# Kernel optimization log

Measured on AMD Instinct MI355X. Metric: run time of the kernel, lower is better.

## Reference

```python
import jax, jax.numpy as jnp
import numpy as np

NUM_ITERATIONS = 3


def squash(t, axis=-1):
    # scale * t / ||t||, scale = ||t||^2 / (1 + ||t||^2)
    sq = jnp.sum(t * t, axis=axis, keepdims=True)
    return (sq / (1.0 + sq)) * t / jnp.sqrt(sq)


def setup_inputs() -> dict:
    key = jax.random.key(0)
    k1, k2 = jax.random.split(key)
    B, N_IN, IN_DIM = 32, 2048, 32
    N_OUT, OUT_DIM = 64, 32
    x = jax.random.normal(k1, (B, N_IN, IN_DIM), dtype=jnp.float32)
    weight = jax.random.normal(k2, (N_OUT, N_IN, OUT_DIM, IN_DIM), dtype=jnp.float32) * 0.05
    return {"x": x, "weight": weight}


def reference(x, weight):
    # u_hat[b,o,i,d] = sum_k W[o,i,d,k] * x[b,i,k]  -- prediction vectors
    u_hat = jnp.einsum('oidk,bik->boid', weight, x)  # [B, N_out, N_in, out_dim]
    b = jnp.zeros(u_hat.shape[:3] + (1,), dtype=u_hat.dtype)  # routing logits
    v = None
    for _ in range(NUM_ITERATIONS):
        c = jax.nn.softmax(b, axis=1)                      # over output capsules
        s = jnp.sum(c * u_hat, axis=2, keepdims=True)      # [B, N_out, 1, out_dim]
        v = squash(s, axis=-1)
        b = b + jnp.sum(u_hat * v, axis=-1, keepdims=True)  # agreement update
    return jnp.squeeze(v, axis=2)  # [B, N_out, out_dim]
```

## Files before the change

### kernel.cpp

```cpp
#include <hip/hip_runtime.h>

#define NI   2048
#define NO   64
#define DD   32
#define ODIM 2048

typedef short bf16x8 __attribute__((ext_vector_type(8)));
typedef float f32x4  __attribute__((ext_vector_type(4)));
typedef unsigned int u32x2 __attribute__((ext_vector_type(2)));
typedef unsigned int u32x4 __attribute__((ext_vector_type(4)));

__device__ __forceinline__ unsigned int cvt_pk_bf16(float lo, float hi) {
  unsigned int r;
  asm("v_cvt_pk_bf16_f32 %0, %1, %2" : "=v"(r) : "v"(lo), "v"(hi));
  return r;
}
__device__ __forceinline__ float bflo(unsigned int u) { return __uint_as_float(u << 16); }
__device__ __forceinline__ float bfhi(unsigned int u) { return __uint_as_float(u & 0xffff0000u); }

union BFPack { unsigned int u[4]; bf16x8 v; };

__global__ __launch_bounds__(256) void k1_uhat(
    const float* __restrict__ W, const float* __restrict__ X,
    unsigned short* __restrict__ U, float* __restrict__ part) {
  __shared__ __attribute__((aligned(16))) char olds[8 * 32 * 144];
  __shared__ __attribute__((aligned(16))) unsigned short xlds[8][32][32];
  const int tid   = threadIdx.x;
  const int lane  = tid & 63;
  const int w     = tid >> 6;
  const int ob    = blockIdx.x & 31;
  const int ib    = blockIdx.x >> 5;
  const int odq   = (ob << 2) + w;
  const int o     = odq >> 1;
  const int db    = (odq & 1) << 4;
  const int row16 = lane & 15;
  const int kg    = lane >> 4;
  const int k0    = kg << 3;
  const int crow  = kg << 2;
  const int ccol  = lane & 15;
  const int odl   = (w << 4) + crow;
  const int sb    = tid >> 3;
  const int sii   = tid & 7;
  const int xslot = (kg ^ (ccol & 3)) << 3;

  f32x4 sacc[2];
  sacc[0] = f32x4{0.f, 0.f, 0.f, 0.f};
  sacc[1] = f32x4{0.f, 0.f, 0.f, 0.f};

  const float* wbase = W + (((size_t)o * NI) << 10) + ((db + row16) << 5) + k0;

  auto STAGE = [&](int p) {
    const int i = (ib << 5) + (p << 3) + sii;
    const float4* xp = (const float4*)(X + (((size_t)(sb * NI + i)) << 5));
    float4 xv[8];
#pragma unroll
    for (int j = 0; j < 8; ++j) xv[j] = xp[j];
#pragma unroll
    for (int j = 0; j < 4; ++j) {
      u32x4 pk;
      pk.x = cvt_pk_bf16(xv[2*j].x,   xv[2*j].y);
      pk.y = cvt_pk_bf16(xv[2*j].z,   xv[2*j].w);
      pk.z = cvt_pk_bf16(xv[2*j+1].x, xv[2*j+1].y);
      pk.w = cvt_pk_bf16(xv[2*j+1].z, xv[2*j+1].w);
      *(u32x4*)&xlds[sii][sb][(j ^ (sb & 3)) << 3] = pk;
    }
  };

  auto ISSUE = [&](int p, int h, f32x4* wa, f32x4* wb) {
    const int ia = (ib << 5) + (p << 3) + (h << 2);
#pragma unroll
    for (int j = 0; j < 4; ++j) {
      const f32x4* wp = (const f32x4*)(wbase + ((size_t)(ia + j) << 10));
      wa[j] = __builtin_nontemporal_load(wp);
      wb[j] = __builtin_nontemporal_load(wp + 1);
    }
    __builtin_amdgcn_sched_barrier(0);
  };

  auto CONSUME = [&](int h, const f32x4* wa, const f32x4* wb) {
#pragma unroll
    for (int j = 0; j < 4; ++j) {
      const int ii = (h << 2) + j;
      bf16x8 bx0 = *(const bf16x8*)&xlds[ii][ccol][xslot];
      bf16x8 bx1 = *(const bf16x8*)&xlds[ii][ccol + 16][xslot];
      BFPack af;
      af.u[0] = cvt_pk_bf16(wa[j].x, wa[j].y);
      af.u[1] = cvt_pk_bf16(wa[j].z, wa[j].w);
      af.u[2] = cvt_pk_bf16(wb[j].x, wb[j].y);
      af.u[3] = cvt_pk_bf16(wb[j].z, wb[j].w);
      {
        f32x4 d = __builtin_amdgcn_mfma_f32_16x16x32_bf16(
            af.v, bx0, f32x4{0.f, 0.f, 0.f, 0.f}, 0, 0, 0);
        sacc[0] += d;
        u32x2 pk; pk.x = cvt_pk_bf16(d[0], d[1]); pk.y = cvt_pk_bf16(d[2], d[3]);
        *(u32x2*)(olds + ((ii << 5) + ccol) * 144 + (odl << 1)) = pk;
      }
      {
        f32x4 d = __builtin_amdgcn_mfma_f32_16x16x32_bf16(
            af.v, bx1, f32x4{0.f, 0.f, 0.f, 0.f}, 0, 0, 0);
        sacc[1] += d;
        u32x2 pk; pk.x = cvt_pk_bf16(d[0], d[1]); pk.y = cvt_pk_bf16(d[2], d[3]);
        *(u32x2*)(olds + ((ii << 5) + ccol + 16) * 144 + (odl << 1)) = pk;
      }
    }
  };

  f32x4 wa0[4], wb0[4], wa1[4], wb1[4];
  STAGE(0);
  ISSUE(0, 0, wa0, wb0);
  __syncthreads();

  for (int p = 0; p < 4; ++p) {
    const int i0 = (ib << 5) + (p << 3);
    ISSUE(p, 1, wa1, wb1);
    CONSUME(0, wa0, wb0);
    if (p < 3) ISSUE(p + 1, 0, wa0, wb0);
    CONSUME(1, wa1, wb1);
    __syncthreads();
    if (p < 3) STAGE(p + 1);
    {
      const int b    = tid >> 3;
      const int od16 = tid & 7;
#pragma unroll
      for (int r = 0; r < 8; ++r) {
        const u32x4 v = *(const u32x4*)(olds + ((r << 5) + b) * 144 + (od16 << 4));
        const size_t goff = (((size_t)(b * NI + i0 + r)) << 11) + (ob << 6) + (od16 << 3);
        *(u32x4*)(U + goff) = v;
      }
    }
    __syncthreads();
  }

#pragma unroll
  for (int bt = 0; bt < 2; ++bt) {
    const int b  = ccol + (bt << 4);
    const int od = (ob << 6) + odl;
    float* pp = part + (((size_t)((ib << 5) + b)) << 11) + od;
    float4 t; t.x = sacc[bt][0]; t.y = sacc[bt][1];
    t.z = sacc[bt][2]; t.w = sacc[bt][3];
    *(float4*)pp = t;
  }
}

__global__ __launch_bounds__(256) void k_reduce(
    const float* __restrict__ part, float* __restrict__ vout, float scale) {
  const int tid  = threadIdx.x;
  const int lane = tid & 63;
  const int wid  = (blockIdx.x << 2) + (tid >> 6);
  const int o = wid & 63, b = wid >> 6;
  const int d = lane & 31, h = lane >> 5;
  float s = 0.f;
  for (int c = h; c < 64; c += 2)
    s += part[(((size_t)((c << 5) + b)) << 11) + (o << 5) + d];
  s += __shfl_xor(s, 32);
  s *= scale;
  float p = s * s;
#pragma unroll
  for (int off = 1; off < 32; off <<= 1) p += __shfl_xor(p, off);
  const float v = (p > 0.f) ? s * sqrtf(p) / (1.f + p) : 0.f;
  if (h == 0) vout[(((b << 6) + o) << 5) + d] = v;
}

__global__ __launch_bounds__(256) void k_route(
    const unsigned short* __restrict__ U, const float* __restrict__ V1,
    const float* __restrict__ V2, float* __restrict__ part) {
  __shared__ float red[4][ODIM];
  const int tid   = threadIdx.x;
  const int lane  = tid & 63;
  const int w     = tid >> 6;
  const int b     = blockIdx.x >> 6;
  const int chunk = blockIdx.x & 63;
  const int o     = lane;

  float vs[32];
  {
    const float* vp = V1 + (((b << 6) + o) << 5);
#pragma unroll
    for (int j = 0; j < 8; ++j) {
      const float4 t = *(const float4*)(vp + (j << 2));
      vs[4*j+0] = t.x; vs[4*j+1] = t.y; vs[4*j+2] = t.z; vs[4*j+3] = t.w;
    }
    if (V2 != nullptr) {
      const float* vq = V2 + (((b << 6) + o) << 5);
#pragma unroll
      for (int j = 0; j < 8; ++j) {
        const float4 t = *(const float4*)(vq + (j << 2));
        vs[4*j+0] += t.x; vs[4*j+1] += t.y; vs[4*j+2] += t.z; vs[4*j+3] += t.w;
      }
    }
  }

  float pacc[32];
#pragma unroll
  for (int d = 0; d < 32; ++d) pacc[d] = 0.f;

  const int i0 = (chunk << 5) + (w << 3);
  const unsigned short* ub = U + (((size_t)b * NI) << 11);

  u32x4 q0, q1, q2, q3;
  {
    const u32x4* p = (const u32x4*)(ub + (((size_t)i0) << 11) + (o << 5));
    q0 = p[0]; q1 = p[1]; q2 = p[2]; q3 = p[3];
  }
  for (int ii = 0; ii < 8; ++ii) {
    const u32x4 c0 = q0, c1 = q1, c2 = q2, c3 = q3;
    if (ii < 7) {
      const u32x4* p = (const u32x4*)(ub + (((size_t)(i0 + ii + 1)) << 11) + (o << 5));
      q0 = p[0]; q1 = p[1]; q2 = p[2]; q3 = p[3];
    }
    float uf[32];
    uf[ 0]=bflo(c0.x); uf[ 1]=bfhi(c0.x); uf[ 2]=bflo(c0.y); uf[ 3]=bfhi(c0.y);
    uf[ 4]=bflo(c0.z); uf[ 5]=bfhi(c0.z); uf[ 6]=bflo(c0.w); uf[ 7]=bfhi(c0.w);
    uf[ 8]=bflo(c1.x); uf[ 9]=bfhi(c1.x); uf[10]=bflo(c1.y); uf[11]=bfhi(c1.y);
    uf[12]=bflo(c1.z); uf[13]=bfhi(c1.z); uf[14]=bflo(c1.w); uf[15]=bfhi(c1.w);
    uf[16]=bflo(c2.x); uf[17]=bfhi(c2.x); uf[18]=bflo(c2.y); uf[19]=bfhi(c2.y);
    uf[20]=bflo(c2.z); uf[21]=bfhi(c2.z); uf[22]=bflo(c2.w); uf[23]=bfhi(c2.w);
    uf[24]=bflo(c3.x); uf[25]=bfhi(c3.x); uf[26]=bflo(c3.y); uf[27]=bfhi(c3.y);
    uf[28]=bflo(c3.z); uf[29]=bfhi(c3.z); uf[30]=bflo(c3.w); uf[31]=bfhi(c3.w);

    float dotA = 0.f, dotB = 0.f;
#pragma unroll
    for (int d = 0; d < 16; ++d) {
      dotA = fmaf(uf[d], vs[d], dotA);
      dotB = fmaf(uf[d + 16], vs[d + 16], dotB);
    }
    const float dot = dotA + dotB;
    float m = dot;
#pragma unroll
    for (int off = 1; off < 64; off <<= 1) m = fmaxf(m, __shfl_xor(m, off));
    const float e = __expf(dot - m);
    float Z = e;
#pragma unroll
    for (int off = 1; off < 64; off <<= 1) Z += __shfl_xor(Z, off);
    const float c = e / Z;
#pragma unroll
    for (int d = 0; d < 32; ++d) pacc[d] = fmaf(c, uf[d], pacc[d]);
  }

#pragma unroll
  for (int j = 0; j < 8; ++j) {
    float4 t; t.x = pacc[4*j]; t.y = pacc[4*j+1]; t.z = pacc[4*j+2]; t.w = pacc[4*j+3];
    *(float4*)&red[w][(o << 5) + (j << 2)] = t;
  }
  __syncthreads();
  float* pout = part + (((size_t)((chunk << 5) + b)) << 11);
  for (int t = tid; t < ODIM; t += 256)
    pout[t] = red[0][t] + red[1][t] + red[2][t] + red[3][t];
}

extern "C" void kernel_launch(void* const* d_in, const int* in_sizes, int n_in,
                              void* d_out, int out_size, void* d_ws, size_t ws_size,
                              hipStream_t stream) {
  const float* X = (const float*)d_in[0];
  const float* W = (const float*)d_in[1];
  float* out = (float*)d_out;
  char* ws = (char*)d_ws;

  unsigned short* U = (unsigned short*)ws;
  float* part = (float*)(ws + ((size_t)268435456));
  float* v1   = (float*)(ws + ((size_t)268435456 + 16777216));
  float* v2   = v1 + 65536;

  k1_uhat<<<2048, 256, 0, stream>>>(W, X, U, part);
  k_reduce<<<512, 256, 0, stream>>>(part, v1, 1.f / 64.f);
  k_route<<<2048, 256, 0, stream>>>(U, v1, nullptr, part);
  k_reduce<<<512, 256, 0, stream>>>(part, v2, 1.f);
  k_route<<<2048, 256, 0, stream>>>(U, v1, v2, part);
  k_reduce<<<512, 256, 0, stream>>>(part, out, 1.f);
}
```

Baseline: 328.1 us.

## Write u_hat straight to global and double-buffer x staging in LDS

Removes the LDS staging buffer for the bf16 u_hat tile, so each lane writes its 8-byte MFMA result fragment directly to global memory instead of going through shared memory and issuing coalesced 16-byte stores. It also double-buffers the x tile in LDS so the next stage is loaded before the current compute, which drops one barrier per iteration. The trade-off is more scattered, smaller global stores with worse coalescing, in exchange for less LDS traffic and fewer synchronisations.

```diff
diff --git a/kernel.cpp b/kernel.cpp
--- a/kernel.cpp
+++ b/kernel.cpp
@@ -23,8 +23,7 @@
 __global__ __launch_bounds__(256) void k1_uhat(
     const float* __restrict__ W, const float* __restrict__ X,
     unsigned short* __restrict__ U, float* __restrict__ part) {
-  __shared__ __attribute__((aligned(16))) char olds[8 * 32 * 144];
-  __shared__ __attribute__((aligned(16))) unsigned short xlds[8][32][32];
+  __shared__ __attribute__((aligned(16))) unsigned short xlds[2][8][32][32];
   const int tid   = threadIdx.x;
   const int lane  = tid & 63;
   const int w     = tid >> 6;
@@ -38,10 +37,10 @@
   const int k0    = kg << 3;
   const int crow  = kg << 2;
   const int ccol  = lane & 15;
-  const int odl   = (w << 4) + crow;
   const int sb    = tid >> 3;
   const int sii   = tid & 7;
   const int xslot = (kg ^ (ccol & 3)) << 3;
+  const int od    = (odq << 4) + crow;
 
   f32x4 sacc[2];
   sacc[0] = f32x4{0.f, 0.f, 0.f, 0.f};
@@ -49,7 +48,7 @@
 
   const float* wbase = W + (((size_t)o * NI) << 10) + ((db + row16) << 5) + k0;
 
-  auto STAGE = [&](int p) {
+  auto STAGE = [&](int p, int buf) {
     const int i = (ib << 5) + (p << 3) + sii;
     const float4* xp = (const float4*)(X + (((size_t)(sb * NI + i)) << 5));
     float4 xv[8];
@@ -62,7 +61,7 @@
       pk.y = cvt_pk_bf16(xv[2*j].z,   xv[2*j].w);
       pk.z = cvt_pk_bf16(xv[2*j+1].x, xv[2*j+1].y);
       pk.w = cvt_pk_bf16(xv[2*j+1].z, xv[2*j+1].w);
-      *(u32x4*)&xlds[sii][sb][(j ^ (sb & 3)) << 3] = pk;
+      *(u32x4*)&xlds[buf][sii][sb][(j ^ (sb & 3)) << 3] = pk;
     }
   };
 
@@ -77,12 +76,13 @@
     __builtin_amdgcn_sched_barrier(0);
   };
 
-  auto CONSUME = [&](int h, const f32x4* wa, const f32x4* wb) {
+  auto CONSUME = [&](int p, int buf, int h, const f32x4* wa, const f32x4* wb) {
 #pragma unroll
     for (int j = 0; j < 4; ++j) {
       const int ii = (h << 2) + j;
-      bf16x8 bx0 = *(const bf16x8*)&xlds[ii][ccol][xslot];
-      bf16x8 bx1 = *(const bf16x8*)&xlds[ii][ccol + 16][xslot];
+      const int i  = (ib << 5) + (p << 3) + ii;
+      bf16x8 bx0 = *(const bf16x8*)&xlds[buf][ii][ccol][xslot];
+      bf16x8 bx1 = *(const bf16x8*)&xlds[buf][ii][ccol + 16][xslot];
       BFPack af;
       af.u[0] = cvt_pk_bf16(wa[j].x, wa[j].y);
       af.u[1] = cvt_pk_bf16(wa[j].z, wa[j].w);
@@ -93,49 +93,38 @@
             af.v, bx0, f32x4{0.f, 0.f, 0.f, 0.f}, 0, 0, 0);
         sacc[0] += d;
         u32x2 pk; pk.x = cvt_pk_bf16(d[0], d[1]); pk.y = cvt_pk_bf16(d[2], d[3]);
-        *(u32x2*)(olds + ((ii << 5) + ccol) * 144 + (odl << 1)) = pk;
+        *(u32x2*)(U + (((size_t)(ccol * NI + i)) << 11) + od) = pk;
       }
       {
         f32x4 d = __builtin_amdgcn_mfma_f32_16x16x32_bf16(
             af.v, bx1, f32x4{0.f, 0.f, 0.f, 0.f}, 0, 0, 0);
         sacc[1] += d;
         u32x2 pk; pk.x = cvt_pk_bf16(d[0], d[1]); pk.y = cvt_pk_bf16(d[2], d[3]);
-        *(u32x2*)(olds + ((ii << 5) + ccol + 16) * 144 + (odl << 1)) = pk;
+        *(u32x2*)(U + (((size_t)((ccol + 16) * NI + i)) << 11) + od) = pk;
       }
     }
   };
 
   f32x4 wa0[4], wb0[4], wa1[4], wb1[4];
-  STAGE(0);
+  STAGE(0, 0);
   ISSUE(0, 0, wa0, wb0);
   __syncthreads();
 
   for (int p = 0; p < 4; ++p) {
-    const int i0 = (ib << 5) + (p << 3);
+    const int buf = p & 1;
+    if (p < 3) STAGE(p + 1, buf ^ 1);
     ISSUE(p, 1, wa1, wb1);
-    CONSUME(0, wa0, wb0);
+    CONSUME(p, buf, 0, wa0, wb0);
     if (p < 3) ISSUE(p + 1, 0, wa0, wb0);
-    CONSUME(1, wa1, wb1);
+    CONSUME(p, buf, 1, wa1, wb1);
     __syncthreads();
-    if (p < 3) STAGE(p + 1);
-    {
-      const int b    = tid >> 3;
-      const int od16 = tid & 7;
-#pragma unroll
-      for (int r = 0; r < 8; ++r) {
-        const u32x4 v = *(const u32x4*)(olds + ((r << 5) + b) * 144 + (od16 << 4));
-        const size_t goff = (((size_t)(b * NI + i0 + r)) << 11) + (ob << 6) + (od16 << 3);
-        *(u32x4*)(U + goff) = v;
-      }
-    }
-    __syncthreads();
   }
 
 #pragma unroll
   for (int bt = 0; bt < 2; ++bt) {
-    const int b  = ccol + (bt << 4);
-    const int od = (ob << 6) + odl;
-    float* pp = part + (((size_t)((ib << 5) + b)) << 11) + od;
+    const int b = ccol + (bt << 4);
+    float* pp = part + (((size_t)((ib << 5) + b)) << 11) + (ob << 6)
+              + ((w << 4) + crow);
     float4 t; t.x = sacc[bt][0]; t.y = sacc[bt][1];
     t.z = sacc[bt][2]; t.w = sacc[bt][3];
     *(float4*)pp = t;
```

Result: slower. 376.7 us (+14.8%).
